# Kernel tuning notes

Hardware: AMD Instinct MI355X
Metric: run time of the kernel (lower is better)

The kernel has to match this reference:

```python
import jax, jax.numpy as jnp
import numpy as np

N = 50000   # nodes
E = 800000  # edges (before self-loops)
IN = 128    # input feature dim
H = 4       # attention heads


def setup_inputs() -> dict:
    key = jax.random.key(0)
    ks = jax.random.split(key, 32)
    f = lambda k, s: (jax.random.normal(k, s, dtype=jnp.float32) * 0.1)
    inp = {
        "x": jax.random.normal(ks[0], (N, IN), dtype=jnp.float32),
        "edge_index": jax.random.randint(ks[1], (2, E), 0, N, dtype=jnp.int32),
        "edge_attr": jax.random.normal(ks[2], (E, 1), dtype=jnp.float32),
        # GATConv 1: 128 -> 8 per head, 4 heads (concat -> 32)
        "W1": f(ks[3], (IN, 32)), "as1": f(ks[4], (H, 8)), "ad1": f(ks[5], (H, 8)), "b1": jnp.zeros((32,), jnp.float32),
        # GATConv 2: 32 -> 16 per head (concat -> 64)
        "W2": f(ks[6], (32, 64)), "as2": f(ks[7], (H, 16)), "ad2": f(ks[8], (H, 16)), "b2": jnp.zeros((64,), jnp.float32),
        # GATConv 3: 64 -> 32 per head (concat -> 128)
        "W3": f(ks[9], (64, 128)), "as3": f(ks[10], (H, 32)), "ad3": f(ks[11], (H, 32)), "b3": jnp.zeros((128,), jnp.float32),
        # GATConv 4: 128 -> 64 per head (concat -> 256)
        "W4": f(ks[12], (128, 256)), "as4": f(ks[13], (H, 64)), "ad4": f(ks[14], (H, 64)), "b4": jnp.zeros((256,), jnp.float32),
        # MLP head
        "Wr": f(ks[15], (256, 32)), "br": jnp.zeros((32,), jnp.float32),
        "Wf1": f(ks[16], (32, 64)), "bf1": jnp.zeros((64,), jnp.float32),
        "Wf2": f(ks[17], (64, 1)), "bf2": jnp.zeros((1,), jnp.float32),
    }
    return inp


def _gat_layer(x, W, a_src, a_dst, bias, src, dst):
    """PyG GATConv (concat=True, negative_slope=0.2, self-loops appended upstream)."""
    heads, C = a_src.shape
    h = (x @ W).reshape(-1, heads, C)              # [N, H, C]
    alpha_s = jnp.sum(h * a_src[None], axis=-1)    # [N, H]
    alpha_d = jnp.sum(h * a_dst[None], axis=-1)    # [N, H]
    e = jax.nn.leaky_relu(alpha_s[src] + alpha_d[dst], 0.2)  # [E', H]
    # segment softmax over incoming edges of each destination node
    emax = jax.ops.segment_max(e, dst, num_segments=N)
    ee = jnp.exp(e - emax[dst])
    denom = jax.ops.segment_sum(ee, dst, num_segments=N)
    alpha = ee / denom[dst]                        # [E', H]
    msg = h[src] * alpha[:, :, None]               # [E', H, C]
    out = jax.ops.segment_sum(msg, dst, num_segments=N)  # [N, H, C]
    return out.reshape(-1, heads * C) + bias


def reference(x, edge_index, edge_attr,
              W1, as1, ad1, b1, W2, as2, ad2, b2,
              W3, as3, ad3, b3, W4, as4, ad4, b4,
              Wr, br, Wf1, bf1, Wf2, bf2):
    # edge_attr is accepted but unused, matching the original forward.
    loop = jnp.arange(N, dtype=edge_index.dtype)
    src = jnp.concatenate([edge_index[0], loop])   # add self-loops (PyG default)
    dst = jnp.concatenate([edge_index[1], loop])
    h = jax.nn.elu(_gat_layer(x, W1, as1, ad1, b1, src, dst))
    h = jax.nn.elu(_gat_layer(h, W2, as2, ad2, b2, src, dst))
    h = jax.nn.elu(_gat_layer(h, W3, as3, ad3, b3, src, dst))
    h = jax.nn.elu(_gat_layer(h, W4, as4, ad4, b4, src, dst))
    h = jax.nn.elu(h @ Wr + br)
    h = jax.nn.elu(h @ Wf1 + bf1)
    return h @ Wf2 + bf2                           # [N, 1]
```

## Files before the change

kernel.cpp:

```cpp
#include <hip/hip_runtime.h>
#include <hip/hip_fp16.h>
#include <math.h>

constexpr int NN = 50000;
constexpr int NE = 800000;
constexpr int NEP = NE + NN;
constexpr int CAP = 96;
constexpr int SCAT_B = (NEP + 255) / 256;

typedef _Float16 half8_t __attribute__((ext_vector_type(8)));
typedef float    f32x4_t __attribute__((ext_vector_type(4)));

__device__ __forceinline__ float lrelu02(float x) { return x > 0.f ? x : 0.2f * x; }
__device__ __forceinline__ float eluf(float x)    { return x > 0.f ? x : (__expf(x) - 1.f); }
__device__ __forceinline__ float pick4(float4 q, int hd) {
  return (hd == 0) ? q.x : (hd == 1) ? q.y : (hd == 2) ? q.z : q.w;
}


__device__ __forceinline__ void pack_w_one(const float* __restrict__ W,
                                           __half* __restrict__ Wp,
                                           int M, int tid, int total) {
  if (tid >= total) return;
  int CT = M >> 4;
  int l = tid & 63;
  int c = (tid >> 6) % CT;
  int kc = (tid >> 6) / CT;
  int n = l & 15, q = l >> 4;
  __half* dst = Wp + (size_t)tid * 8;
  const float* src = W + (size_t)(kc * 32 + q * 8) * M + c * 16 + n;
  #pragma unroll
  for (int j = 0; j < 8; j++) dst[j] = __float2half_rn(src[j * M]);
}


__global__ __launch_bounds__(256) void scatter_pack_kernel(
    const int* __restrict__ edge_src, const int* __restrict__ edge_dst,
    int* __restrict__ count, int* __restrict__ csr_src,
    const float* __restrict__ W1, __half* __restrict__ Wp1,
    const float* __restrict__ W2, __half* __restrict__ Wp2,
    const float* __restrict__ W3, __half* __restrict__ Wp3,
    const float* __restrict__ W4, __half* __restrict__ Wp4,
    const float* __restrict__ Wr, __half* __restrict__ Wrp,
    const float* __restrict__ Wf1, __half* __restrict__ Wf1p) {
  int b = blockIdx.x;
  if (b < SCAT_B) {
    int i = b * 256 + threadIdx.x;
    if (i < NEP) {
      int s, d;
      if (i < NE) { s = edge_src[i]; d = edge_dst[i]; } else { s = i - NE; d = s; }
      int pos = atomicAdd(&count[d], 1);
      if (pos < CAP) csr_src[d * CAP + pos] = s;
    }
  } else {
    int tid = (b - SCAT_B) * 256 + threadIdx.x;
    if (tid < 512)            pack_w_one(W1, Wp1, 32,  tid,        512);
    else if (tid < 768)       pack_w_one(W2, Wp2, 64,  tid - 512,  256);
    else if (tid < 1792)      pack_w_one(W3, Wp3, 128, tid - 768,  1024);
    else if (tid < 5888)      pack_w_one(W4, Wp4, 256, tid - 1792, 4096);
    else if (tid < 6912)      pack_w_one(Wr, Wrp, 32,  tid - 5888, 1024);
    else if (tid < 7168)      pack_w_one(Wf1, Wf1p, 64, tid - 6912, 256);
  }
}


template<int M, int C, int CT>
__device__ __forceinline__ void alpha_epilogue(const f32x4_t* acc,
    const float* __restrict__ a_src, const float* __restrict__ a_dst,
    int row_base, int m, float* __restrict__ as_out, float* __restrict__ ad_out) {
  float aS[CT], aD[CT];
  #pragma unroll
  for (int c = 0; c < CT; c++) { aS[c] = a_src[c * 16 + m]; aD[c] = a_dst[c * 16 + m]; }

  if constexpr (C == 8) {
    #pragma unroll
    for (int r = 0; r < 4; r++) {
      float p0 = acc[0][r] * aS[0], p1 = acc[1][r] * aS[1];
      float q0 = acc[0][r] * aD[0], q1 = acc[1][r] * aD[1];
      #pragma unroll
      for (int off = 1; off < 8; off <<= 1) {
        p0 += __shfl_xor(p0, off); p1 += __shfl_xor(p1, off);
        q0 += __shfl_xor(q0, off); q1 += __shfl_xor(q1, off);
      }
      int row = row_base + r;
      if ((m & 7) == 0 && row < NN) {
        int hb = m >> 3;
        as_out[row * 4 + hb]     = p0;
        as_out[row * 4 + 2 + hb] = p1;
        ad_out[row * 4 + hb]     = q0;
        ad_out[row * 4 + 2 + hb] = q1;
      }
    }
  } else {
    constexpr int FPH = C / 16;
    #pragma unroll
    for (int r = 0; r < 4; r++) {
      float bs[4] = {0.f, 0.f, 0.f, 0.f}, bd[4] = {0.f, 0.f, 0.f, 0.f};
      #pragma unroll
      for (int c = 0; c < CT; c++) {
        int hd = c / FPH;
        bs[hd] += acc[c][r] * aS[c];
        bd[hd] += acc[c][r] * aD[c];
      }
      #pragma unroll
      for (int off = 1; off < 16; off <<= 1)
        #pragma unroll
        for (int h = 0; h < 4; h++) {
          bs[h] += __shfl_xor(bs[h], off);
          bd[h] += __shfl_xor(bd[h], off);
        }
      int row = row_base + r;
      if (m < 4 && row < NN) {
        float vs = (m == 0) ? bs[0] : (m == 1) ? bs[1] : (m == 2) ? bs[2] : bs[3];
        float vd = (m == 0) ? bd[0] : (m == 1) ? bd[1] : (m == 2) ? bd[2] : bd[3];
        as_out[row * 4 + m] = vs;
        ad_out[row * 4 + m] = vd;
      }
    }
  }
}


template<int M, int K, int C>
__global__ __launch_bounds__(256) void gemm_mfma_f32_kernel(const float* __restrict__ A,
    const __half* __restrict__ Wp, __half* __restrict__ Ch,
    const float* __restrict__ a_src, const float* __restrict__ a_dst,
    float* __restrict__ as_out, float* __restrict__ ad_out) {
  constexpr int CT = M / 16;
  constexpr int KC = K / 32;
  __shared__ _Float16 Ah[64 * 40];
  int t = threadIdx.x;
  int w = t >> 6, l = t & 63;
  int m = l & 15, q = l >> 4;
  int row0 = blockIdx.x * 64;

  f32x4_t acc[CT];
  #pragma unroll
  for (int c = 0; c < CT; c++) acc[c] = (f32x4_t){0.f, 0.f, 0.f, 0.f};

  const half8_t* Bfrag = (const half8_t*)Wp;

  for (int kc = 0; kc < KC; kc++) {
    __syncthreads();
    #pragma unroll
    for (int i = 0; i < 2; i++) {
      int idx = t + 256 * i;
      int row = idx >> 3, c4 = idx & 7;
      int gr = row0 + row; if (gr >= NN) gr = NN - 1;
      float4 v = *(const float4*)(A + (size_t)gr * K + kc * 32 + c4 * 4);
      _Float16 h[4] = {(_Float16)v.x, (_Float16)v.y, (_Float16)v.z, (_Float16)v.w};
      *(uint2*)(&Ah[row * 40 + c4 * 4]) = *(const uint2*)h;
    }
    __syncthreads();
    half8_t a = *(const half8_t*)(&Ah[(w * 16 + m) * 40 + q * 8]);
    #pragma unroll
    for (int c = 0; c < CT; c++) {
      half8_t b = Bfrag[(kc * CT + c) * 64 + l];
      acc[c] = __builtin_amdgcn_mfma_f32_16x16x32_f16(a, b, acc[c], 0, 0, 0);
    }
  }

  #pragma unroll
  for (int r = 0; r < 4; r++) {
    int row = row0 + w * 16 + q * 4 + r;
    if (row < NN) {
      #pragma unroll
      for (int c = 0; c < CT; c++)
        Ch[(size_t)row * M + c * 16 + m] = __float2half_rn(acc[c][r]);
    }
  }
  alpha_epilogue<M, C, CT>(acc, a_src, a_dst, row0 + w * 16 + q * 4, m, as_out, ad_out);
}


template<int M, int K, int C>
__global__ __launch_bounds__(256) void gemm_mfma_f16_kernel(const __half* __restrict__ A,
    const __half* __restrict__ Wp, __half* __restrict__ Ch,
    const float* __restrict__ a_src, const float* __restrict__ a_dst,
    float* __restrict__ as_out, float* __restrict__ ad_out) {
  constexpr int CT = M / 16;
  constexpr int KC = K / 32;
  __shared__ _Float16 Ah[64 * 40];
  int t = threadIdx.x;
  int w = t >> 6, l = t & 63;
  int m = l & 15, q = l >> 4;
  int row0 = blockIdx.x * 64;

  f32x4_t acc[CT];
  #pragma unroll
  for (int c = 0; c < CT; c++) acc[c] = (f32x4_t){0.f, 0.f, 0.f, 0.f};

  const half8_t* Bfrag = (const half8_t*)Wp;

  for (int kc = 0; kc < KC; kc++) {
    __syncthreads();
    {
      int row = t >> 2, c8 = t & 3;
      int gr = row0 + row; if (gr >= NN) gr = NN - 1;
      uint4 v = *(const uint4*)(A + (size_t)gr * K + kc * 32 + c8 * 8);
      *(uint4*)(&Ah[row * 40 + c8 * 8]) = v;
    }
    __syncthreads();
    half8_t a = *(const half8_t*)(&Ah[(w * 16 + m) * 40 + q * 8]);
    #pragma unroll
    for (int c = 0; c < CT; c++) {
      half8_t b = Bfrag[(kc * CT + c) * 64 + l];
      acc[c] = __builtin_amdgcn_mfma_f32_16x16x32_f16(a, b, acc[c], 0, 0, 0);
    }
  }

  #pragma unroll
  for (int r = 0; r < 4; r++) {
    int row = row0 + w * 16 + q * 4 + r;
    if (row < NN) {
      #pragma unroll
      for (int c = 0; c < CT; c++)
        Ch[(size_t)row * M + c * 16 + m] = __float2half_rn(acc[c][r]);
    }
  }
  alpha_epilogue<M, C, CT>(acc, a_src, a_dst, row0 + w * 16 + q * 4, m, as_out, ad_out);
}


template<int HC, int C>
__global__ __launch_bounds__(256) void agg_kernel(const __half* __restrict__ h,
    const float* __restrict__ as_v, const float* __restrict__ ad_v,
    const int* __restrict__ count, const int* __restrict__ csr_src,
    const float* __restrict__ bias, __half* __restrict__ out) {
  constexpr int V = HC / 8;
  constexpr int G = 64 / V;
  constexpr int P = 4;
  __shared__ float4 see4[4][CAP];
  __shared__ int    ssrc[4][CAP];
  int wid = threadIdx.x >> 6, lane = threadIdx.x & 63;
  int dst = blockIdx.x * 4 + wid;
  int base = dst * CAP;
  int deg = count[dst]; if (deg > CAP) deg = CAP;
  float4 ad = *(const float4*)(ad_v + dst * 4);

  float d0 = 0.f, d1 = 0.f, d2 = 0.f, d3 = 0.f;
  #pragma unroll
  for (int it = 0; it < 2; it++) {
    int j = lane + it * 64;
    if (j < deg) {
      int s = csr_src[base + j];
      float4 as = *(const float4*)(as_v + s * 4);
      float4 x = make_float4(__expf(lrelu02(as.x + ad.x)), __expf(lrelu02(as.y + ad.y)),
                             __expf(lrelu02(as.z + ad.z)), __expf(lrelu02(as.w + ad.w)));
      ssrc[wid][j] = s; see4[wid][j] = x;
      d0 += x.x; d1 += x.y; d2 += x.z; d3 += x.w;
    }
  }
  #pragma unroll
  for (int off = 32; off > 0; off >>= 1) {
    d0 += __shfl_xor(d0, off); d1 += __shfl_xor(d1, off);
    d2 += __shfl_xor(d2, off); d3 += __shfl_xor(d3, off);
  }
  float4 inv = make_float4(1.f / d0, 1.f / d1, 1.f / d2, 1.f / d3);

  int g = lane / V, v = lane % V;
  int hd = (v * 8) / C;
  float invh = pick4(inv, hd);
  int steps = (deg + G - 1) / G;
  const float4* hrows = (const float4*)h;

  float  px[P];
  float4 hv[P];
  #pragma unroll
  for (int k = 0; k < P; k++) {
    int jj = k * G + g;
    bool ok = jj < deg;
    int jc = ok ? jj : 0;
    int s = ssrc[wid][jc];
    float x = ((const float*)&see4[wid][jc])[hd];
    px[k] = ok ? x * invh : 0.f;
    hv[k] = hrows[(size_t)s * V + v];
  }

  float acc[8];
  #pragma unroll
  for (int i = 0; i < 8; i++) acc[i] = 0.f;
  int nB = (steps + P - 1) / P;
  for (int b = 1; b <= nB; b++) {
    #pragma unroll
    for (int k = 0; k < P; k++) {
      const __half2* hp = (const __half2*)&hv[k];
      float2 f0 = __half22float2(hp[0]);
      float2 f1 = __half22float2(hp[1]);
      float2 f2 = __half22float2(hp[2]);
      float2 f3 = __half22float2(hp[3]);
      float p = px[k];
      acc[0] += p * f0.x; acc[1] += p * f0.y;
      acc[2] += p * f1.x; acc[3] += p * f1.y;
      acc[4] += p * f2.x; acc[5] += p * f2.y;
      acc[6] += p * f3.x; acc[7] += p * f3.y;
      int jj = (b * P + k) * G + g;
      bool ok = jj < deg;
      int jc = ok ? jj : 0;
      int s = ssrc[wid][jc];
      float x = ((const float*)&see4[wid][jc])[hd];
      px[k] = ok ? x * invh : 0.f;
      hv[k] = hrows[(size_t)s * V + v];
    }
  }

  #pragma unroll
  for (int off = V; off < 64; off <<= 1)
    #pragma unroll
    for (int i = 0; i < 8; i++) acc[i] += __shfl_xor(acc[i], off);

  if (lane < V) {
    const float4* b4 = (const float4*)bias;
    float4 ba = b4[2 * v], bb = b4[2 * v + 1];
    _Float16 o[8];
    o[0] = (_Float16)eluf(acc[0] + ba.x); o[1] = (_Float16)eluf(acc[1] + ba.y);
    o[2] = (_Float16)eluf(acc[2] + ba.z); o[3] = (_Float16)eluf(acc[3] + ba.w);
    o[4] = (_Float16)eluf(acc[4] + bb.x); o[5] = (_Float16)eluf(acc[5] + bb.y);
    o[6] = (_Float16)eluf(acc[6] + bb.z); o[7] = (_Float16)eluf(acc[7] + bb.w);
    *(uint4*)(out + (size_t)dst * HC + v * 8) = *(const uint4*)o;
  }
}


__global__ __launch_bounds__(256) void mlp_mfma_kernel(const __half* __restrict__ h4,
    const __half* __restrict__ Wrp, const float* __restrict__ br,
    const __half* __restrict__ Wf1p, const float* __restrict__ bf1,
    const float* __restrict__ Wf2, const float* __restrict__ bf2,
    float* __restrict__ out) {
  __shared__ _Float16 rS[64 * 40];
  int t = threadIdx.x;
  int w = t >> 6, l = t & 63;
  int m = l & 15, q = l >> 4;
  int row0 = blockIdx.x * 64;
  const half8_t* Bwr  = (const half8_t*)Wrp;
  const half8_t* Bwf1 = (const half8_t*)Wf1p;

  int arow = row0 + w * 16 + m; if (arow >= NN) arow = NN - 1;
  const half8_t* Arow = (const half8_t*)(h4 + (size_t)arow * 256);
  half8_t afr[8];
  #pragma unroll
  for (int kc = 0; kc < 8; kc++) afr[kc] = Arow[kc * 4 + q];
  f32x4_t acc1[2];
  acc1[0] = (f32x4_t){0.f, 0.f, 0.f, 0.f};
  acc1[1] = (f32x4_t){0.f, 0.f, 0.f, 0.f};
  #pragma unroll
  for (int kc = 0; kc < 8; kc++) {
    acc1[0] = __builtin_amdgcn_mfma_f32_16x16x32_f16(afr[kc], Bwr[(kc * 2 + 0) * 64 + l], acc1[0], 0, 0, 0);
    acc1[1] = __builtin_amdgcn_mfma_f32_16x16x32_f16(afr[kc], Bwr[(kc * 2 + 1) * 64 + l], acc1[1], 0, 0, 0);
  }
  #pragma unroll
  for (int c = 0; c < 2; c++)
    #pragma unroll
    for (int r = 0; r < 4; r++) {
      float vv = eluf(acc1[c][r] + br[c * 16 + m]);
      rS[(w * 16 + q * 4 + r) * 40 + c * 16 + m] = (_Float16)vv;
    }
  __syncthreads();

  half8_t a2 = *(const half8_t*)(&rS[(w * 16 + m) * 40 + q * 8]);
  f32x4_t acc2[4];
  #pragma unroll
  for (int c = 0; c < 4; c++) acc2[c] = (f32x4_t){0.f, 0.f, 0.f, 0.f};
  #pragma unroll
  for (int c = 0; c < 4; c++)
    acc2[c] = __builtin_amdgcn_mfma_f32_16x16x32_f16(a2, Bwf1[c * 64 + l], acc2[c], 0, 0, 0);

  float wv[4] = {Wf2[m], Wf2[16 + m], Wf2[32 + m], Wf2[48 + m]};
  float rsum[4];
  #pragma unroll
  for (int r = 0; r < 4; r++) {
    float sr = 0.f;
    #pragma unroll
    for (int c = 0; c < 4; c++)
      sr += eluf(acc2[c][r] + bf1[c * 16 + m]) * wv[c];
    #pragma unroll
    for (int off = 1; off < 16; off <<= 1) sr += __shfl_xor(sr, off);
    rsum[r] = sr;
  }
  if (m == 0) {
    float b = bf2[0];
    #pragma unroll
    for (int r = 0; r < 4; r++) {
      int row = row0 + w * 16 + q * 4 + r;
      if (row < NN) out[row] = rsum[r] + b;
    }
  }
}


extern "C" void kernel_launch(void* const* d_in, const int* in_sizes, int n_in,
                              void* d_out, int out_size, void* d_ws, size_t ws_size,
                              hipStream_t stream) {
  const float* x   = (const float*)d_in[0];
  const int*   ei  = (const int*)d_in[1];
  const float* W1  = (const float*)d_in[3];
  const float* as1 = (const float*)d_in[4];
  const float* ad1 = (const float*)d_in[5];
  const float* b1  = (const float*)d_in[6];
  const float* W2  = (const float*)d_in[7];
  const float* as2 = (const float*)d_in[8];
  const float* ad2 = (const float*)d_in[9];
  const float* b2  = (const float*)d_in[10];
  const float* W3  = (const float*)d_in[11];
  const float* as3 = (const float*)d_in[12];
  const float* ad3 = (const float*)d_in[13];
  const float* b3  = (const float*)d_in[14];
  const float* W4  = (const float*)d_in[15];
  const float* as4 = (const float*)d_in[16];
  const float* ad4 = (const float*)d_in[17];
  const float* b4  = (const float*)d_in[18];
  const float* Wr  = (const float*)d_in[19];
  const float* br  = (const float*)d_in[20];
  const float* Wf1 = (const float*)d_in[21];
  const float* bf1 = (const float*)d_in[22];
  const float* Wf2 = (const float*)d_in[23];
  const float* bf2 = (const float*)d_in[24];
  float* out = (float*)d_out;

  char* p = (char*)d_ws;
  auto alloc = [&](size_t bytes) {
    char* q = p;
    p += (bytes + 255) & ~(size_t)255;
    return q;
  };
  int* count   = (int*)alloc((size_t)NN * 4);
  int* csr_src = (int*)alloc((size_t)NN * CAP * 4);
  __half* Hh = (__half*)alloc((size_t)NN * 256 * 2);
  __half* B2 = (__half*)alloc((size_t)NN * 128 * 2);
  __half* B3 = (__half*)alloc((size_t)NN * 256 * 2);
  float* as_buf = (float*)alloc((size_t)NN * 4 * 4);
  float* ad_buf = (float*)alloc((size_t)NN * 4 * 4);
  __half* Wp1 = (__half*)alloc((size_t)128 * 32 * 2);
  __half* Wp2 = (__half*)alloc((size_t)32 * 64 * 2);
  __half* Wp3 = (__half*)alloc((size_t)64 * 128 * 2);
  __half* Wp4 = (__half*)alloc((size_t)128 * 256 * 2);
  __half* Wrp = (__half*)alloc((size_t)256 * 32 * 2);
  __half* Wf1p = (__half*)alloc((size_t)32 * 64 * 2);

  const int* edge_src = ei;
  const int* edge_dst = ei + NE;

  hipMemsetAsync(count, 0, (size_t)NN * 4, stream);
  scatter_pack_kernel<<<SCAT_B + 28, 256, 0, stream>>>(
      edge_src, edge_dst, count, csr_src,
      W1, Wp1, W2, Wp2, W3, Wp3, W4, Wp4, Wr, Wrp, Wf1, Wf1p);

  int gb  = (NN + 63) / 64;
  int ggb = NN / 4;

  gemm_mfma_f32_kernel<32, 128, 8><<<gb, 256, 0, stream>>>(x, Wp1, Hh, as1, ad1, as_buf, ad_buf);
  agg_kernel<32, 8><<<ggb, 256, 0, stream>>>(Hh, as_buf, ad_buf, count, csr_src, b1, B2);

  gemm_mfma_f16_kernel<64, 32, 16><<<gb, 256, 0, stream>>>(B2, Wp2, Hh, as2, ad2, as_buf, ad_buf);
  agg_kernel<64, 16><<<ggb, 256, 0, stream>>>(Hh, as_buf, ad_buf, count, csr_src, b2, B3);

  gemm_mfma_f16_kernel<128, 64, 32><<<gb, 256, 0, stream>>>(B3, Wp3, Hh, as3, ad3, as_buf, ad_buf);
  agg_kernel<128, 32><<<ggb, 256, 0, stream>>>(Hh, as_buf, ad_buf, count, csr_src, b3, B2);

  gemm_mfma_f16_kernel<256, 128, 64><<<gb, 256, 0, stream>>>(B2, Wp4, Hh, as4, ad4, as_buf, ad_buf);
  agg_kernel<256, 64><<<ggb, 256, 0, stream>>>(Hh, as_buf, ad_buf, count, csr_src, b4, B3);

  mlp_mfma_kernel<<<gb, 256, 0, stream>>>(B3, Wrp, br, Wf1p, bf1, Wf2, bf2, out);
}
```

Measured before the change: 403.8 us.

## Fuse GAT aggregation with next layer's GEMM and MLP head via LDS

```diff
diff --git a/kernel.cpp b/kernel.cpp
--- a/kernel.cpp
+++ b/kernel.cpp
@@ -173,128 +173,51 @@
 }
 
 
-template<int M, int K, int C>
-__global__ __launch_bounds__(256) void gemm_mfma_f16_kernel(const __half* __restrict__ A,
-    const __half* __restrict__ Wp, __half* __restrict__ Ch,
-    const float* __restrict__ a_src, const float* __restrict__ a_dst,
-    float* __restrict__ as_out, float* __restrict__ ad_out) {
-  constexpr int CT = M / 16;
-  constexpr int KC = K / 32;
-  __shared__ _Float16 Ah[64 * 40];
-  int t = threadIdx.x;
-  int w = t >> 6, l = t & 63;
-  int m = l & 15, q = l >> 4;
-  int row0 = blockIdx.x * 64;
-
-  f32x4_t acc[CT];
-  #pragma unroll
-  for (int c = 0; c < CT; c++) acc[c] = (f32x4_t){0.f, 0.f, 0.f, 0.f};
-
-  const half8_t* Bfrag = (const half8_t*)Wp;
-
-  for (int kc = 0; kc < KC; kc++) {
-    __syncthreads();
-    {
-      int row = t >> 2, c8 = t & 3;
-      int gr = row0 + row; if (gr >= NN) gr = NN - 1;
-      uint4 v = *(const uint4*)(A + (size_t)gr * K + kc * 32 + c8 * 8);
-      *(uint4*)(&Ah[row * 40 + c8 * 8]) = v;
-    }
-    __syncthreads();
-    half8_t a = *(const half8_t*)(&Ah[(w * 16 + m) * 40 + q * 8]);
-    #pragma unroll
-    for (int c = 0; c < CT; c++) {
-      half8_t b = Bfrag[(kc * CT + c) * 64 + l];
-      acc[c] = __builtin_amdgcn_mfma_f32_16x16x32_f16(a, b, acc[c], 0, 0, 0);
-    }
-  }
-
-  #pragma unroll
-  for (int r = 0; r < 4; r++) {
-    int row = row0 + w * 16 + q * 4 + r;
-    if (row < NN) {
-      #pragma unroll
-      for (int c = 0; c < CT; c++)
-        Ch[(size_t)row * M + c * 16 + m] = __float2half_rn(acc[c][r]);
-    }
-  }
-  alpha_epilogue<M, C, CT>(acc, a_src, a_dst, row0 + w * 16 + q * 4, m, as_out, ad_out);
-}
-
-
-template<int HC, int C>
-__global__ __launch_bounds__(256) void agg_kernel(const __half* __restrict__ h,
+template<int HC, int C, int STR>
+__device__ __forceinline__ void agg_phase(const __half* __restrict__ h,
     const float* __restrict__ as_v, const float* __restrict__ ad_v,
     const int* __restrict__ count, const int* __restrict__ csr_src,
-    const float* __restrict__ bias, __half* __restrict__ out) {
+    const float* __restrict__ bias, _Float16* __restrict__ Ah,
+    float4 (*see4)[CAP], int (*ssrc)[CAP], int row0, int wid, int lane) {
   constexpr int V = HC / 8;
   constexpr int G = 64 / V;
   constexpr int P = 4;
-  __shared__ float4 see4[4][CAP];
-  __shared__ int    ssrc[4][CAP];
-  int wid = threadIdx.x >> 6, lane = threadIdx.x & 63;
-  int dst = blockIdx.x * 4 + wid;
-  int base = dst * CAP;
-  int deg = count[dst]; if (deg > CAP) deg = CAP;
-  float4 ad = *(const float4*)(ad_v + dst * 4);
-
-  float d0 = 0.f, d1 = 0.f, d2 = 0.f, d3 = 0.f;
-  #pragma unroll
-  for (int it = 0; it < 2; it++) {
-    int j = lane + it * 64;
-    if (j < deg) {
-      int s = csr_src[base + j];
-      float4 as = *(const float4*)(as_v + s * 4);
-      float4 x = make_float4(__expf(lrelu02(as.x + ad.x)), __expf(lrelu02(as.y + ad.y)),
-                             __expf(lrelu02(as.z + ad.z)), __expf(lrelu02(as.w + ad.w)));
-      ssrc[wid][j] = s; see4[wid][j] = x;
-      d0 += x.x; d1 += x.y; d2 += x.z; d3 += x.w;
-    }
-  }
-  #pragma unroll
-  for (int off = 32; off > 0; off >>= 1) {
-    d0 += __shfl_xor(d0, off); d1 += __shfl_xor(d1, off);
-    d2 += __shfl_xor(d2, off); d3 += __shfl_xor(d3, off);
-  }
-  float4 inv = make_float4(1.f / d0, 1.f / d1, 1.f / d2, 1.f / d3);
-
   int g = lane / V, v = lane % V;
   int hd = (v * 8) / C;
-  float invh = pick4(inv, hd);
-  int steps = (deg + G - 1) / G;
   const float4* hrows = (const float4*)h;
 
-  float  px[P];
-  float4 hv[P];
-  #pragma unroll
-  for (int k = 0; k < P; k++) {
-    int jj = k * G + g;
-    bool ok = jj < deg;
-    int jc = ok ? jj : 0;
-    int s = ssrc[wid][jc];
-    float x = ((const float*)&see4[wid][jc])[hd];
-    px[k] = ok ? x * invh : 0.f;
-    hv[k] = hrows[(size_t)s * V + v];
-  }
-
-  float acc[8];
-  #pragma unroll
-  for (int i = 0; i < 8; i++) acc[i] = 0.f;
-  int nB = (steps + P - 1) / P;
-  for (int b = 1; b <= nB; b++) {
+  for (int n = 0; n < 16; n++) {
+    int dst = row0 + wid * 16 + n; if (dst >= NN) dst = NN - 1;
+    int base = dst * CAP;
+    int deg = count[dst]; if (deg > CAP) deg = CAP;
+    float4 ad = *(const float4*)(ad_v + dst * 4);
+
+    float d0 = 0.f, d1 = 0.f, d2 = 0.f, d3 = 0.f;
+    #pragma unroll
+    for (int it = 0; it < 2; it++) {
+      int j = lane + it * 64;
+      if (j < deg) {
+        int s = csr_src[base + j];
+        float4 as = *(const float4*)(as_v + s * 4);
+        float4 x = make_float4(__expf(lrelu02(as.x + ad.x)), __expf(lrelu02(as.y + ad.y)),
+                               __expf(lrelu02(as.z + ad.z)), __expf(lrelu02(as.w + ad.w)));
+        ssrc[wid][j] = s; see4[wid][j] = x;
+        d0 += x.x; d1 += x.y; d2 += x.z; d3 += x.w;
+      }
+    }
+    #pragma unroll
+    for (int off = 32; off > 0; off >>= 1) {
+      d0 += __shfl_xor(d0, off); d1 += __shfl_xor(d1, off);
+      d2 += __shfl_xor(d2, off); d3 += __shfl_xor(d3, off);
+    }
+    float4 inv4 = make_float4(1.f / d0, 1.f / d1, 1.f / d2, 1.f / d3);
+    float invh = pick4(inv4, hd);
+
+    float  px[P];
+    float4 hv[P];
     #pragma unroll
     for (int k = 0; k < P; k++) {
-      const __half2* hp = (const __half2*)&hv[k];
-      float2 f0 = __half22float2(hp[0]);
-      float2 f1 = __half22float2(hp[1]);
-      float2 f2 = __half22float2(hp[2]);
-      float2 f3 = __half22float2(hp[3]);
-      float p = px[k];
-      acc[0] += p * f0.x; acc[1] += p * f0.y;
-      acc[2] += p * f1.x; acc[3] += p * f1.y;
-      acc[4] += p * f2.x; acc[5] += p * f2.y;
-      acc[6] += p * f3.x; acc[7] += p * f3.y;
-      int jj = (b * P + k) * G + g;
+      int jj = k * G + g;
       bool ok = jj < deg;
       int jc = ok ? jj : 0;
       int s = ssrc[wid][jc];
@@ -302,68 +225,150 @@
       px[k] = ok ? x * invh : 0.f;
       hv[k] = hrows[(size_t)s * V + v];
     }
-  }
-
-  #pragma unroll
-  for (int off = V; off < 64; off <<= 1)
-    #pragma unroll
-    for (int i = 0; i < 8; i++) acc[i] += __shfl_xor(acc[i], off);
-
-  if (lane < V) {
-    const float4* b4 = (const float4*)bias;
-    float4 ba = b4[2 * v], bb = b4[2 * v + 1];
-    _Float16 o[8];
-    o[0] = (_Float16)eluf(acc[0] + ba.x); o[1] = (_Float16)eluf(acc[1] + ba.y);
-    o[2] = (_Float16)eluf(acc[2] + ba.z); o[3] = (_Float16)eluf(acc[3] + ba.w);
-    o[4] = (_Float16)eluf(acc[4] + bb.x); o[5] = (_Float16)eluf(acc[5] + bb.y);
-    o[6] = (_Float16)eluf(acc[6] + bb.z); o[7] = (_Float16)eluf(acc[7] + bb.w);
-    *(uint4*)(out + (size_t)dst * HC + v * 8) = *(const uint4*)o;
-  }
-}
-
-
-__global__ __launch_bounds__(256) void mlp_mfma_kernel(const __half* __restrict__ h4,
+    float acc[8];
+    #pragma unroll
+    for (int i = 0; i < 8; i++) acc[i] = 0.f;
+    int steps = (deg + G - 1) / G;
+    int nB = (steps + P - 1) / P;
+    for (int b = 1; b <= nB; b++) {
+      #pragma unroll
+      for (int k = 0; k < P; k++) {
+        const __half2* hp = (const __half2*)&hv[k];
+        float2 f0 = __half22float2(hp[0]);
+        float2 f1 = __half22float2(hp[1]);
+        float2 f2 = __half22float2(hp[2]);
+        float2 f3 = __half22float2(hp[3]);
+        float p = px[k];
+        acc[0] += p * f0.x; acc[1] += p * f0.y;
+        acc[2] += p * f1.x; acc[3] += p * f1.y;
+        acc[4] += p * f2.x; acc[5] += p * f2.y;
+        acc[6] += p * f3.x; acc[7] += p * f3.y;
+        int jj = (b * P + k) * G + g;
+        bool ok = jj < deg;
+        int jc = ok ? jj : 0;
+        int s = ssrc[wid][jc];
+        float x = ((const float*)&see4[wid][jc])[hd];
+        px[k] = ok ? x * invh : 0.f;
+        hv[k] = hrows[(size_t)s * V + v];
+      }
+    }
+    #pragma unroll
+    for (int off = V; off < 64; off <<= 1)
+      #pragma unroll
+      for (int i = 0; i < 8; i++) acc[i] += __shfl_xor(acc[i], off);
+
+    if (lane < V) {
+      const float4* b4p = (const float4*)bias;
+      float4 ba = b4p[2 * v], bb = b4p[2 * v + 1];
+      _Float16 o[8];
+      o[0] = (_Float16)eluf(acc[0] + ba.x); o[1] = (_Float16)eluf(acc[1] + ba.y);
+      o[2] = (_Float16)eluf(acc[2] + ba.z); o[3] = (_Float16)eluf(acc[3] + ba.w);
+      o[4] = (_Float16)eluf(acc[4] + bb.x); o[5] = (_Float16)eluf(acc[5] + bb.y);
+      o[6] = (_Float16)eluf(acc[6] + bb.z); o[7] = (_Float16)eluf(acc[7] + bb.w);
+      *(uint4*)(&Ah[(wid * 16 + n) * STR + v * 8]) = *(const uint4*)o;
+    }
+  }
+}
+
+
+template<int HC, int C, int M>
+__global__ __launch_bounds__(256) void agg_gemm_kernel(const __half* __restrict__ h,
+    const float* __restrict__ as_v, const float* __restrict__ ad_v,
+    const int* __restrict__ count, const int* __restrict__ csr_src,
+    const float* __restrict__ bias,
+    const __half* __restrict__ Wp, __half* __restrict__ Ch,
+    const float* __restrict__ a_src, const float* __restrict__ a_dst,
+    float* __restrict__ as_out, float* __restrict__ ad_out) {
+  constexpr int STR = HC + 8;
+  constexpr int CT = M / 16;
+  constexpr int KC = HC / 32;
+  __shared__ float4 see4[4][CAP];
+  __shared__ int    ssrc[4][CAP];
+  __shared__ _Float16 Ah[64 * STR];
+  int t = threadIdx.x, wid = t >> 6, lane = t & 63;
+  int row0 = blockIdx.x * 64;
+
+  agg_phase<HC, C, STR>(h, as_v, ad_v, count, csr_src, bias, Ah, see4, ssrc, row0, wid, lane);
+  __syncthreads();
+
+  int m = lane & 15, q = lane >> 4;
+  f32x4_t gacc[CT];
+  #pragma unroll
+  for (int c = 0; c < CT; c++) gacc[c] = (f32x4_t){0.f, 0.f, 0.f, 0.f};
+  const half8_t* Bfrag = (const half8_t*)Wp;
+  #pragma unroll
+  for (int kc = 0; kc < KC; kc++) {
+    half8_t a = *(const half8_t*)(&Ah[(wid * 16 + m) * STR + kc * 32 + q * 8]);
+    #pragma unroll
+    for (int c = 0; c < CT; c++) {
+      half8_t b = Bfrag[(kc * CT + c) * 64 + lane];
+      gacc[c] = __builtin_amdgcn_mfma_f32_16x16x32_f16(a, b, gacc[c], 0, 0, 0);
+    }
+  }
+  #pragma unroll
+  for (int r = 0; r < 4; r++) {
+    int row = row0 + wid * 16 + q * 4 + r;
+    if (row < NN) {
+      #pragma unroll
+      for (int c = 0; c < CT; c++)
+        Ch[(size_t)row * M + c * 16 + m] = __float2half_rn(gacc[c][r]);
+    }
+  }
+  alpha_epilogue<M, M / 4, CT>(gacc, a_src, a_dst, row0 + wid * 16 + q * 4, m, as_out, ad_out);
+}
+
+
+__global__ __launch_bounds__(256) void agg_mlp_kernel(const __half* __restrict__ h,
+    const float* __restrict__ as_v, const float* __restrict__ ad_v,
+    const int* __restrict__ count, const int* __restrict__ csr_src,
+    const float* __restrict__ bias,
     const __half* __restrict__ Wrp, const float* __restrict__ br,
     const __half* __restrict__ Wf1p, const float* __restrict__ bf1,
     const float* __restrict__ Wf2, const float* __restrict__ bf2,
     float* __restrict__ out) {
+  constexpr int STR = 264;
+  __shared__ float4 see4[4][CAP];
+  __shared__ int    ssrc[4][CAP];
+  __shared__ _Float16 Ah[64 * STR];
   __shared__ _Float16 rS[64 * 40];
-  int t = threadIdx.x;
-  int w = t >> 6, l = t & 63;
-  int m = l & 15, q = l >> 4;
+  int t = threadIdx.x, wid = t >> 6, lane = t & 63;
   int row0 = blockIdx.x * 64;
+
+  agg_phase<256, 64, STR>(h, as_v, ad_v, count, csr_src, bias, Ah, see4, ssrc, row0, wid, lane);
+  __syncthreads();
+
+  int m = lane & 15, q = lane >> 4;
   const half8_t* Bwr  = (const half8_t*)Wrp;
   const half8_t* Bwf1 = (const half8_t*)Wf1p;
 
-  int arow = row0 + w * 16 + m; if (arow >= NN) arow = NN - 1;
-  const half8_t* Arow = (const half8_t*)(h4 + (size_t)arow * 256);
   half8_t afr[8];
   #pragma unroll
-  for (int kc = 0; kc < 8; kc++) afr[kc] = Arow[kc * 4 + q];
+  for (int kc = 0; kc < 8; kc++)
+    afr[kc] = *(const half8_t*)(&Ah[(wid * 16 + m) * STR + kc * 32 + q * 8]);
   f32x4_t acc1[2];
   acc1[0] = (f32x4_t){0.f, 0.f, 0.f, 0.f};
   acc1[1] = (f32x4_t){0.f, 0.f, 0.f, 0.f};
   #pragma unroll
   for (int kc = 0; kc < 8; kc++) {
-    acc1[0] = __builtin_amdgcn_mfma_f32_16x16x32_f16(afr[kc], Bwr[(kc * 2 + 0) * 64 + l], acc1[0], 0, 0, 0);
-    acc1[1] = __builtin_amdgcn_mfma_f32_16x16x32_f16(afr[kc], Bwr[(kc * 2 + 1) * 64 + l], acc1[1], 0, 0, 0);
+    acc1[0] = __builtin_amdgcn_mfma_f32_16x16x32_f16(afr[kc], Bwr[(kc * 2 + 0) * 64 + lane], acc1[0], 0, 0, 0);
+    acc1[1] = __builtin_amdgcn_mfma_f32_16x16x32_f16(afr[kc], Bwr[(kc * 2 + 1) * 64 + lane], acc1[1], 0, 0, 0);
   }
   #pragma unroll
   for (int c = 0; c < 2; c++)
     #pragma unroll
     for (int r = 0; r < 4; r++) {
       float vv = eluf(acc1[c][r] + br[c * 16 + m]);
-      rS[(w * 16 + q * 4 + r) * 40 + c * 16 + m] = (_Float16)vv;
+      rS[(wid * 16 + q * 4 + r) * 40 + c * 16 + m] = (_Float16)vv;
     }
   __syncthreads();
 
-  half8_t a2 = *(const half8_t*)(&rS[(w * 16 + m) * 40 + q * 8]);
+  half8_t a2 = *(const half8_t*)(&rS[(wid * 16 + m) * 40 + q * 8]);
   f32x4_t acc2[4];
   #pragma unroll
   for (int c = 0; c < 4; c++) acc2[c] = (f32x4_t){0.f, 0.f, 0.f, 0.f};
   #pragma unroll
   for (int c = 0; c < 4; c++)
-    acc2[c] = __builtin_amdgcn_mfma_f32_16x16x32_f16(a2, Bwf1[c * 64 + l], acc2[c], 0, 0, 0);
+    acc2[c] = __builtin_amdgcn_mfma_f32_16x16x32_f16(a2, Bwf1[c * 64 + lane], acc2[c], 0, 0, 0);
 
   float wv[4] = {Wf2[m], Wf2[16 + m], Wf2[32 + m], Wf2[48 + m]};
   float rsum[4];
@@ -381,7 +386,7 @@
     float b = bf2[0];
     #pragma unroll
     for (int r = 0; r < 4; r++) {
-      int row = row0 + w * 16 + q * 4 + r;
+      int row = row0 + wid * 16 + q * 4 + r;
       if (row < NN) out[row] = rsum[r] + b;
     }
   }
@@ -425,11 +430,12 @@
   };
   int* count   = (int*)alloc((size_t)NN * 4);
   int* csr_src = (int*)alloc((size_t)NN * CAP * 4);
-  __half* Hh = (__half*)alloc((size_t)NN * 256 * 2);
-  __half* B2 = (__half*)alloc((size_t)NN * 128 * 2);
-  __half* B3 = (__half*)alloc((size_t)NN * 256 * 2);
-  float* as_buf = (float*)alloc((size_t)NN * 4 * 4);
-  float* ad_buf = (float*)alloc((size_t)NN * 4 * 4);
+  __half* HhA = (__half*)alloc((size_t)NN * 128 * 2);
+  __half* HhB = (__half*)alloc((size_t)NN * 256 * 2);
+  float* as_a = (float*)alloc((size_t)NN * 4 * 4);
+  float* ad_a = (float*)alloc((size_t)NN * 4 * 4);
+  float* as_b = (float*)alloc((size_t)NN * 4 * 4);
+  float* ad_b = (float*)alloc((size_t)NN * 4 * 4);
   __half* Wp1 = (__half*)alloc((size_t)128 * 32 * 2);
   __half* Wp2 = (__half*)alloc((size_t)32 * 64 * 2);
   __half* Wp3 = (__half*)alloc((size_t)64 * 128 * 2);
@@ -445,20 +451,15 @@
       edge_src, edge_dst, count, csr_src,
       W1, Wp1, W2, Wp2, W3, Wp3, W4, Wp4, Wr, Wrp, Wf1, Wf1p);
 
-  int gb  = (NN + 63) / 64;
-  int ggb = NN / 4;
-
-  gemm_mfma_f32_kernel<32, 128, 8><<<gb, 256, 0, stream>>>(x, Wp1, Hh, as1, ad1, as_buf, ad_buf);
-  agg_kernel<32, 8><<<ggb, 256, 0, stream>>>(Hh, as_buf, ad_buf, count, csr_src, b1, B2);
-
-  gemm_mfma_f16_kernel<64, 32, 16><<<gb, 256, 0, stream>>>(B2, Wp2, Hh, as2, ad2, as_buf, ad_buf);
-  agg_kernel<64, 16><<<ggb, 256, 0, stream>>>(Hh, as_buf, ad_buf, count, csr_src, b2, B3);
-
-  gemm_mfma_f16_kernel<128, 64, 32><<<gb, 256, 0, stream>>>(B3, Wp3, Hh, as3, ad3, as_buf, ad_buf);
-  agg_kernel<128, 32><<<ggb, 256, 0, stream>>>(Hh, as_buf, ad_buf, count, csr_src, b3, B2);
-
-  gemm_mfma_f16_kernel<256, 128, 64><<<gb, 256, 0, stream>>>(B2, Wp4, Hh, as4, ad4, as_buf, ad_buf);
-  agg_kernel<256, 64><<<ggb, 256, 0, stream>>>(Hh, as_buf, ad_buf, count, csr_src, b4, B3);
-
-  mlp_mfma_kernel<<<gb, 256, 0, stream>>>(B3, Wrp, br, Wf1p, bf1, Wf2, bf2, out);
-}
+  int gb = (NN + 63) / 64;
+
+  gemm_mfma_f32_kernel<32, 128, 8><<<gb, 256, 0, stream>>>(x, Wp1, HhA, as1, ad1, as_a, ad_a);
+  agg_gemm_kernel<32, 8, 64><<<gb, 256, 0, stream>>>(
+      HhA, as_a, ad_a, count, csr_src, b1, Wp2, HhB, as2, ad2, as_b, ad_b);
+  agg_gemm_kernel<64, 16, 128><<<gb, 256, 0, stream>>>(
+      HhB, as_b, ad_b, count, csr_src, b2, Wp3, HhA, as3, ad3, as_a, ad_a);
+  agg_gemm_kernel<128, 32, 256><<<gb, 256, 0, stream>>>(
+      HhA, as_a, ad_a, count, csr_src, b3, Wp4, HhB, as4, ad4, as_b, ad_b);
+  agg_mlp_kernel<<<gb, 256, 0, stream>>>(
+      HhB, as_b, ad_b, count, csr_src, b4, Wrp, br, Wf1p, bf1, Wf2, bf2, out);
+}
```

Result: slower. 515.4 us (+27.6%).
